# Kernel optimization log

Hardware: AMD Instinct MI355X
Metric: run time of the kernel (lower is better)

Reference implementation:

```python
import jax, jax.numpy as jnp
import numpy as np


def _rotate_half(x):
    x1, x2 = jnp.split(x, 2, axis=-1)
    return jnp.concatenate((-x2, x1), axis=-1)


def setup_inputs() -> dict:
    key = jax.random.key(0)
    ks = jax.random.split(key, 8)
    B, T, C, H = 2, 2048, 1024, 16
    Dh = C // H
    x = jax.random.normal(ks[0], (B, T, C), dtype=jnp.float32)
    # RoPE tables (T, head_dim)
    inv_freq = 1.0 / (10000.0 ** (np.arange(0, Dh, 2, dtype=np.float32) / Dh))
    pos = np.arange(T, dtype=np.float32)
    freqs = np.einsum('t,f->tf', pos, inv_freq)
    emb = np.concatenate([freqs, freqs], axis=-1)
    cos = jnp.asarray(np.cos(emb), dtype=jnp.float32)
    sin = jnp.asarray(np.sin(emb), dtype=jnp.float32)
    # causal mask: 1 where attending allowed, 0 elsewhere
    mask = jnp.tril(jnp.ones((T, T), dtype=jnp.int32))
    s = 0.02
    Wq = jax.random.normal(ks[1], (C, C), dtype=jnp.float32) * s
    Wk = jax.random.normal(ks[2], (C, C), dtype=jnp.float32) * s
    Wv = jax.random.normal(ks[3], (C, C), dtype=jnp.float32) * s
    Wo = jax.random.normal(ks[4], (C, C), dtype=jnp.float32) * s
    return {"x": x, "cos": cos, "sin": sin, "mask": mask, "n_heads": H,
            "Wq": Wq, "Wk": Wk, "Wv": Wv, "Wo": Wo}


def reference(x, cos, sin, mask, n_heads, Wq, Wk, Wv, Wo):
    B, T, C = x.shape
    H = n_heads
    Dh = C // H
    scale = Dh ** (-0.5)
    # projections (torch Linear: x @ W.T), reshape to (B, H, T, Dh)
    def proj(W):
        return (x @ W.T).reshape(B, T, H, Dh).transpose(0, 2, 1, 3)
    q, k, v = proj(Wq), proj(Wk), proj(Wv)
    # RoPE: cos/sin broadcast as (1, 1, T, Dh)
    c = cos[None, None]
    s = sin[None, None]
    q = q * c + _rotate_half(q) * s
    k = k * c + _rotate_half(k) * s
    att = jnp.einsum('bhtd,bhsd->bhts', q, k) * scale
    att = jnp.where(mask == 0, -jnp.inf, att)
    att = jax.nn.softmax(att, axis=-1)
    out = jnp.einsum('bhts,bhsd->bhtd', att, v)
    out = out.transpose(0, 2, 1, 3).reshape(B, T, C)
    return out @ Wo.T
```

## Files before the change

### kernel.cpp

```cpp
#include <hip/hip_runtime.h>
#include <stdint.h>

#define B_   2
#define T_   2048
#define C_   1024
#define H_   16
#define BT   4096
#define KDIM 1024

typedef unsigned short u16;
typedef __attribute__((ext_vector_type(8))) __bf16 bf16v8;
typedef __attribute__((ext_vector_type(4))) float f32x4;
typedef __attribute__((ext_vector_type(16))) float f32x16;
typedef __attribute__((ext_vector_type(4))) unsigned int u32x4;
typedef __attribute__((ext_vector_type(2))) unsigned int u32x2;

#define MFMA16(a, b, c) __builtin_amdgcn_mfma_f32_16x16x32_bf16((a), (b), (c), 0, 0, 0)
#define MFMA32(a, b, c) __builtin_amdgcn_mfma_f32_32x32x16_bf16((a), (b), (c), 0, 0, 0)

#define BARRIER() do { asm volatile("" ::: "memory"); \
                       __builtin_amdgcn_s_barrier();  \
                       asm volatile("" ::: "memory"); } while (0)

__device__ __forceinline__ u16 f2bf(float f) {
  __bf16 h = (__bf16)f;
  union { __bf16 h; u16 u; } v; v.h = h;
  return v.u;
}
__device__ __forceinline__ float bf2f(u16 u) {
  union { uint32_t u; float f; } v; v.u = (uint32_t)u << 16;
  return v.f;
}

__device__ __forceinline__ void xhalf(uint32_t a, uint32_t b,
                                      uint32_t& lo, uint32_t& hi) {
#if defined(__has_builtin) && __has_builtin(__builtin_amdgcn_permlane32_swap)
  u32x2 r = __builtin_amdgcn_permlane32_swap(a, b, false, false);
  lo = r.x; hi = r.y;
#else
  const bool upper = (threadIdx.x & 32) != 0;
  lo = upper ? __shfl_xor(b, 32) : a;
  hi = upper ? b : __shfl_xor(a, 32);
#endif
}

__device__ __forceinline__ void gload16(const void* g, void* l) {
  __builtin_amdgcn_global_load_lds((__attribute__((address_space(1))) void*)g,
                                   (__attribute__((address_space(3))) void*)l,
                                   16, 0, 0);
}

__global__ __launch_bounds__(256) void cvt_all(
    const float* __restrict__ x,
    const float* __restrict__ wq, const float* __restrict__ wk,
    const float* __restrict__ wv, const float* __restrict__ wo,
    u16* __restrict__ xb, u16* __restrict__ qkv_dst, u16* __restrict__ o_dst) {
  const int bid = blockIdx.x;
  const float* src;
  u16* dst;
  int i;
  if (bid < 4096) {
    src = x; dst = xb;
    i = (bid * 256 + threadIdx.x) * 4;
  } else {
    const int b2 = bid - 4096;
    const int sel = b2 >> 10;
    src = (sel == 0) ? wq : (sel == 1) ? wk : (sel == 2) ? wv : wo;
    dst = (sel < 3) ? (qkv_dst + sel * 1048576) : o_dst;
    i = ((b2 & 1023) * 256 + threadIdx.x) * 4;
  }
  float4 v = *(const float4*)(src + i);
  ushort4 o;
  o.x = f2bf(v.x); o.y = f2bf(v.y); o.z = f2bf(v.z); o.w = f2bf(v.w);
  *(ushort4*)(dst + i) = o;
}

__global__ __launch_bounds__(256, 2) void gemm_qkv32(
    const u16* __restrict__ A, const u16* __restrict__ Bm,
    u16* __restrict__ qo, u16* __restrict__ ko, u16* __restrict__ vt,
    const float* __restrict__ cosT, const float* __restrict__ sinT)
{
  __shared__ __align__(16) char smem[32768];
  const int tid = threadIdx.x;
  const int lane = tid & 63;
  const int w = tid >> 6;
  const int wm = w >> 1, wn = w & 1;
  const int lmod = lane & 15, ldiv = lane >> 4;

  const int x = blockIdx.x & 7;
  const int i = blockIdx.x >> 3;
  const int by = (x >> 1) * 8 + (i % 8);
  const int bx = (x & 1) * 12 + (i / 8);
  const int row0 = by * 128, col0 = bx * 128;

  const int ldst = (tid & 192) * 16;

  auto stage = [&](int buf, int t) {
    const int kb = t * 64;
#pragma unroll
    for (int c = 0; c < 2; ++c) {
      const int chunk = c * 256 + tid;
      const int row = chunk >> 2;
      const int col = ((chunk & 3) * 16) ^ ((row & 3) << 4);
      gload16((const char*)A + (size_t)(row0 + row) * 2048 + kb + col,
              smem + buf * 8192 + c * 4096 + ldst);
      gload16((const char*)Bm + (size_t)(col0 + row) * 2048 + kb + col,
              smem + 16384 + buf * 8192 + c * 4096 + ldst);
    }
  };

  f32x4 acc[4][4] = {};
  stage(0, 0);

  for (int t = 0; t < 32; ++t) {
    const int cur = t & 1;
    BARRIER();
    if (t + 1 < 32) {
      stage(cur ^ 1, t + 1);
      asm volatile("s_waitcnt vmcnt(4)" ::: "memory");
    } else {
      asm volatile("s_waitcnt vmcnt(0)" ::: "memory");
    }
    BARRIER();

    bf16v8 af[4], bfr[4];
#pragma unroll
    for (int mf = 0; mf < 4; ++mf) {
      const int rr = wm * 64 + mf * 16 + lmod;
      af[mf] = *(const bf16v8*)(smem + cur * 8192 + rr * 64 +
                    ((ldiv * 16) ^ ((rr & 3) << 4)));
    }
#pragma unroll
    for (int nf = 0; nf < 4; ++nf) {
      const int rr = wn * 64 + nf * 16 + lmod;
      bfr[nf] = *(const bf16v8*)(smem + 16384 + cur * 8192 + rr * 64 +
                    ((ldiv * 16) ^ ((rr & 3) << 4)));
    }
#pragma unroll
    for (int mf = 0; mf < 4; ++mf)
#pragma unroll
      for (int nf = 0; nf < 4; ++nf)
        acc[mf][nf] = MFMA16(af[mf], bfr[nf], acc[mf][nf]);
  }

  const int nb = col0 + wn * 64;
  const int proj = nb >> 10;
  const int hh = (nb & 1023) >> 6;
  if (proj < 2) {
    u16* dst = proj ? ko : qo;
#pragma unroll
    for (int mf = 0; mf < 4; ++mf) {
#pragma unroll
      for (int r = 0; r < 4; ++r) {
        const int m = row0 + wm * 64 + mf * 16 + ldiv * 4 + r;
        const int b = m >> 11, t = m & 2047;
        u16* drow = dst + ((size_t)(b * H_ + hh) * T_ + t) * 64;
#pragma unroll
        for (int nf = 0; nf < 4; ++nf) {
          const int d = nf * 16 + lmod;
          const float cs = cosT[t * 64 + d];
          const float sn = sinT[t * 64 + d];
          const float other = (nf < 2) ? acc[mf][nf + 2][r] : acc[mf][nf - 2][r];
          float val = (nf < 2) ? (acc[mf][nf][r] * cs - other * sn)
                               : (acc[mf][nf][r] * cs + other * sn);
          if (proj == 0) val *= 0.18033688011112042f;
          drow[d] = f2bf(val);
        }
      }
    }
  } else {
    BARRIER();
    char* scr = smem + w * 8192;
#pragma unroll
    for (int nf = 0; nf < 4; ++nf)
#pragma unroll
      for (int mf = 0; mf < 4; ++mf)
#pragma unroll
        for (int rp = 0; rp < 2; ++rp) {
          const int dd = nf * 16 + lmod;
          const int t0 = mf * 16 + ldiv * 4 + rp * 2;
          const uint32_t pk = (uint32_t)f2bf(acc[mf][nf][rp * 2]) |
                              ((uint32_t)f2bf(acc[mf][nf][rp * 2 + 1]) << 16);
          *(uint32_t*)(scr + ((dd * 128 + t0 * 2) ^ ((dd & 7) << 4))) = pk;
        }
    __syncthreads();
    const int trow = row0 + wm * 64;
    const int bb = trow >> 11, tl = trow & 2047;
#pragma unroll
    for (int j = 0; j < 8; ++j) {
      const int dd = j * 8 + (lane >> 3);
      const int c = lane & 7;
      const u32x4 vv = *(const u32x4*)(scr + ((dd * 128 + c * 16) ^ ((dd & 7) << 4)));
      u16* drow = vt + ((size_t)((bb * H_ + hh) * 64 + dd)) * T_ + tl;
      *(u32x4*)((char*)drow + c * 16) = vv;
    }
  }
}

template<int NN>
__global__ __launch_bounds__(256, 2) void gemm128(
    const u16* __restrict__ A, const u16* __restrict__ Bm,
    float* __restrict__ Cf)
{
  __shared__ __align__(16) u16 As[2][128 * 64];
  __shared__ __align__(16) u16 Bs[2][128 * 64];
  const int tid = threadIdx.x;
  const int lane = tid & 63;
  const int w = tid >> 6;
  const int wm = w >> 1, wn = w & 1;
  const int lmod = lane & 15, ldiv = lane >> 4;

  const int x = blockIdx.x & 7;
  const int i = blockIdx.x >> 3;
  const int by = x * 4 + (i % 4);
  const int bx = i / 4;
  const int row0 = by * 128, col0 = bx * 128;

  const int srow = tid >> 3;
  const int sswz = ((tid & 7) * 16) ^ ((srow & 7) << 4);
  const char* Abase = (const char*)A + (size_t)(row0 + srow) * (KDIM * 2) + sswz;
  const char* Bbase = (const char*)Bm + (size_t)(col0 + srow) * (KDIM * 2) + sswz;
  const int ldst = (tid & 192) * 16;

  auto stage = [&](int buf, int t) {
    const int kb = t * 128;
#pragma unroll
    for (int c = 0; c < 4; ++c)
      gload16(Abase + (size_t)c * 32 * (KDIM * 2) + kb,
              (char*)As[buf] + c * 4096 + ldst);
#pragma unroll
    for (int c = 0; c < 4; ++c)
      gload16(Bbase + (size_t)c * 32 * (KDIM * 2) + kb,
              (char*)Bs[buf] + c * 4096 + ldst);
  };

  f32x4 acc[4][4] = {};
  stage(0, 0);

  for (int t = 0; t < KDIM / 64; ++t) {
    const int cur = t & 1;
    BARRIER();
    if (t + 1 < KDIM / 64) {
      stage(cur ^ 1, t + 1);
      asm volatile("s_waitcnt vmcnt(8)" ::: "memory");
    } else {
      asm volatile("s_waitcnt vmcnt(0)" ::: "memory");
    }
    BARRIER();

    bf16v8 af[4][2], bfr[4][2];
#pragma unroll
    for (int mf = 0; mf < 4; ++mf) {
      const int rr = wm * 64 + mf * 16 + lmod;
#pragma unroll
      for (int kc = 0; kc < 2; ++kc)
        af[mf][kc] = *(const bf16v8*)((const char*)As[cur] + rr * 128 +
                          ((kc * 64 + ldiv * 16) ^ ((rr & 7) << 4)));
    }
#pragma unroll
    for (int nf = 0; nf < 4; ++nf) {
      const int rr = wn * 64 + nf * 16 + lmod;
#pragma unroll
      for (int kc = 0; kc < 2; ++kc)
        bfr[nf][kc] = *(const bf16v8*)((const char*)Bs[cur] + rr * 128 +
                          ((kc * 64 + ldiv * 16) ^ ((rr & 7) << 4)));
    }
#pragma unroll
    for (int kc = 0; kc < 2; ++kc)
#pragma unroll
      for (int mf = 0; mf < 4; ++mf)
#pragma unroll
        for (int nf = 0; nf < 4; ++nf)
          acc[mf][nf] = MFMA16(af[mf][kc], bfr[nf][kc], acc[mf][nf]);
  }

#pragma unroll
  for (int mf = 0; mf < 4; ++mf) {
    const int mbase = row0 + wm * 64 + mf * 16 + ldiv * 4;
#pragma unroll
    for (int nf = 0; nf < 4; ++nf) {
      const int n = col0 + wn * 64 + nf * 16 + lmod;
#pragma unroll
      for (int r = 0; r < 4; ++r)
        Cf[(size_t)(mbase + r) * NN + n] = acc[mf][nf][r];
    }
  }
}

__global__ __launch_bounds__(256, 2) void attn_fwd4(
    const u16* __restrict__ Q, const u16* __restrict__ K,
    const u16* __restrict__ Vt, u16* __restrict__ O,
    u16* __restrict__ part_o, float* __restrict__ pml)
{
  __shared__ __align__(16) u16 Kl[2][64 * 64];
  __shared__ __align__(16) u16 Vl[2][64 * 64];
  static const int rmap[24] = {7, 22, 23, 20, 21, 6, 18, 19, 16, 17, 5, 14,
                               15, 12, 13, 4, 10, 11, 8, 9, 3, 2, 1, 0};
  const int xcd = blockIdx.x & 7;
  const int i   = blockIdx.x >> 3;
  const int bh  = xcd * 4 + (i & 3);
  const int r   = rmap[i >> 2];
  int qb0, t0, t1, sid;
  if (r < 8) {
    qb0 = r * 128; t0 = 0; t1 = 2 * r + 2; sid = -1;
  } else {
    const int s = r - 8;
    const int c = 8 + (s >> 1);
    const int half = s & 1;
    qb0 = c * 128;
    t0 = half * (c + 1); t1 = t0 + (c + 1);
    sid = (bh * 8 + (c - 8)) * 2 + half;
  }

  const int tid = threadIdx.x, lane = tid & 63, w = tid >> 6;
  const int l31 = lane & 31, hi = lane >> 5;
  const int qrow = qb0 + w * 32;

  bf16v8 qf[4];
  {
    const u16* qp = Q + ((size_t)bh * T_ + qrow + l31) * 64 + hi * 8;
    qf[0] = *(const bf16v8*)(qp);
    qf[1] = *(const bf16v8*)(qp + 16);
    qf[2] = *(const bf16v8*)(qp + 32);
    qf[3] = *(const bf16v8*)(qp + 48);
  }

  float m2 = -1e30f, lsum = 0.f;
  f32x16 oacc0 = {}, oacc1 = {};

  const int scolb = (tid & 7) * 16;
  const int ldst = (tid & 192) * 16;

  auto stage = [&](int buf, int t) {
    const int s0 = t << 6;
#pragma unroll
    for (int c = 0; c < 2; ++c) {
      const int row = (c * 256 + tid) >> 3;
      const int sw = scolb ^ ((row & 7) << 4);
      gload16((const char*)(K + ((size_t)bh * T_ + s0 + row) * 64) + sw,
              (char*)Kl[buf] + c * 4096 + ldst);
    }
#pragma unroll
    for (int c = 0; c < 2; ++c) {
      const int row = (c * 256 + tid) >> 3;
      const int sw = scolb ^ ((row & 7) << 4);
      gload16((const char*)(Vt + ((size_t)(bh * 64 + row)) * T_ + s0) + sw,
              (char*)Vl[buf] + c * 4096 + ldst);
    }
  };

  auto substep = [&](int cur, int sub, int s0_sub) {
    bf16v8 kf[4], vf[4];
#pragma unroll
    for (int c = 0; c < 4; ++c) {
      const int row = sub * 32 + l31;
      kf[c] = *(const bf16v8*)((const char*)Kl[cur] + row * 128 +
                  ((c * 32 + hi * 16) ^ ((row & 7) << 4)));
    }
#pragma unroll
    for (int db = 0; db < 2; ++db)
#pragma unroll
      for (int kg = 0; kg < 2; ++kg) {
        const int row = db * 32 + l31;
        vf[db * 2 + kg] = *(const bf16v8*)((const char*)Vl[cur] + row * 128 +
                  ((sub * 64 + kg * 32 + hi * 16) ^ ((row & 7) << 4)));
      }
    f32x16 s = {};
    s = MFMA32(kf[0], qf[0], s);
    s = MFMA32(kf[1], qf[1], s);
    s = MFMA32(kf[2], qf[2], s);
    s = MFMA32(kf[3], qf[3], s);
    if (s0_sub + 31 > qrow) {
#pragma unroll
      for (int r2 = 0; r2 < 16; ++r2) {
        const int key = s0_sub + (r2 & 3) + 8 * (r2 >> 2) + 4 * hi;
        if (key > qrow + l31) s[r2] = -1e30f;
      }
    }
    float t8[8];
#pragma unroll
    for (int r2 = 0; r2 < 8; ++r2) t8[r2] = fmaxf(s[r2], s[r2 + 8]);
    float t4a = fmaxf(t8[0], t8[4]), t4b = fmaxf(t8[1], t8[5]);
    float t4c = fmaxf(t8[2], t8[6]), t4d = fmaxf(t8[3], t8[7]);
    float pmax = fmaxf(fmaxf(t4a, t4b), fmaxf(t4c, t4d));
    {
      uint32_t lo, hh2;
      xhalf(__builtin_bit_cast(uint32_t, pmax), __builtin_bit_cast(uint32_t, pmax), lo, hh2);
      pmax = fmaxf(__builtin_bit_cast(float, lo), __builtin_bit_cast(float, hh2));
    }
    if (!__all(pmax <= m2 + 11.5416f)) {
      const float mnew = fmaxf(m2, pmax);
      const float rs = __builtin_amdgcn_exp2f(m2 - mnew);
      lsum *= rs;
#pragma unroll
      for (int r2 = 0; r2 < 16; ++r2) { oacc0[r2] *= rs; oacc1[r2] *= rs; }
      m2 = mnew;
    }
    float p[16];
#pragma unroll
    for (int r2 = 0; r2 < 16; ++r2) p[r2] = __builtin_amdgcn_exp2f(s[r2] - m2);
    float a8[8];
#pragma unroll
    for (int r2 = 0; r2 < 8; ++r2) a8[r2] = p[r2] + p[r2 + 8];
    float a4a = a8[0] + a8[4], a4b = a8[1] + a8[5];
    float a4c = a8[2] + a8[6], a4d = a8[3] + a8[7];
    float ts = (a4a + a4b) + (a4c + a4d);
    {
      uint32_t lo, hh2;
      xhalf(__builtin_bit_cast(uint32_t, ts), __builtin_bit_cast(uint32_t, ts), lo, hh2);
      ts = __builtin_bit_cast(float, lo) + __builtin_bit_cast(float, hh2);
    }
    lsum += ts;
    uint32_t o[8];
#pragma unroll
    for (int jj = 0; jj < 8; ++jj) {
      const int r0 = 4 * (jj >> 1) + 2 * (jj & 1);
      uint32_t d;
      asm("v_cvt_pk_bf16_f32 %0, %1, %2" : "=v"(d) : "v"(p[r0]), "v"(p[r0 + 1]));
      o[jj] = d;
    }
#pragma unroll
    for (int kg = 0; kg < 2; ++kg) {
      uint32_t f0, f1, f2, f3;
      xhalf(o[4 * kg + 0], o[4 * kg + 2], f0, f2);
      xhalf(o[4 * kg + 1], o[4 * kg + 3], f1, f3);
      u32x4 fr;
      fr.x = f0; fr.y = f1; fr.z = f2; fr.w = f3;
      const bf16v8 pf = __builtin_bit_cast(bf16v8, fr);
      oacc0 = MFMA32(vf[kg], pf, oacc0);
      oacc1 = MFMA32(vf[2 + kg], pf, oacc1);
    }
  };

  stage(0, t0);
  for (int t = t0; t < t1; ++t) {
    const int cur = (t - t0) & 1;
    BARRIER();
    if (t + 1 < t1) {
      stage(cur ^ 1, t + 1);
      asm volatile("s_waitcnt vmcnt(4)" ::: "memory");
    } else {
      asm volatile("s_waitcnt vmcnt(0)" ::: "memory");
    }
    BARRIER();
#pragma unroll
    for (int sub = 0; sub < 2; ++sub) {
      const int s0_sub = t * 64 + sub * 32;
      if (s0_sub <= qrow + 31) substep(cur, sub, s0_sub);
    }
  }

  BARRIER();
  char* scr = (char*)Kl + w * 4096;
  const float inv = (sid < 0) ? (1.f / lsum) : 1.f;
#pragma unroll
  for (int r2 = 0; r2 < 8; ++r2) {
    const int r = r2 * 2;
    const int dd = (r & 3) + 8 * (r >> 2) + 4 * hi;
    const uint32_t pk0 = (uint32_t)f2bf(oacc0[r] * inv) |
                         ((uint32_t)f2bf(oacc0[r + 1] * inv) << 16);
    *(uint32_t*)(scr + ((l31 * 128 + dd * 2) ^ ((l31 & 7) << 4))) = pk0;
    const uint32_t pk1 = (uint32_t)f2bf(oacc1[r] * inv) |
                         ((uint32_t)f2bf(oacc1[r + 1] * inv) << 16);
    *(uint32_t*)(scr + ((l31 * 128 + (dd + 32) * 2) ^ ((l31 & 7) << 4))) = pk1;
  }
  __syncthreads();
  const int qq = lane >> 1, cc = lane & 1;
  if (sid < 0) {
    const int b = bh >> 4, hh = bh & 15;
    u16* orow = O + ((size_t)(b * T_ + qrow + qq)) * C_ + hh * 64 + cc * 32;
#pragma unroll
    for (int jj = 0; jj < 4; ++jj) {
      const u32x4 vv = *(const u32x4*)(scr + ((qq * 128 + cc * 64 + jj * 16) ^ ((qq & 7) << 4)));
      *(u32x4*)((char*)orow + jj * 16) = vv;
    }
  } else {
    u16* prow = part_o + ((size_t)(sid * 128 + w * 32 + qq)) * 64 + cc * 32;
#pragma unroll
    for (int jj = 0; jj < 4; ++jj) {
      const u32x4 vv = *(const u32x4*)(scr + ((qq * 128 + cc * 64 + jj * 16) ^ ((qq & 7) << 4)));
      *(u32x4*)((char*)prow + jj * 16) = vv;
    }
    if (lane < 32) {
      pml[sid * 256 + w * 32 + lane] = m2;
      pml[sid * 256 + 128 + w * 32 + lane] = lsum;
    }
  }
}

__global__ __launch_bounds__(256) void attn_combine(
    const u16* __restrict__ part_o, const float* __restrict__ pml,
    u16* __restrict__ O)
{
  const int combo = blockIdx.x;
  const int bh = combo >> 3, c8 = combo & 7;
  const int sid0 = (bh * 8 + c8) * 2;
  const int row = threadIdx.x >> 1, dh = threadIdx.x & 1;
  const float m0 = pml[sid0 * 256 + row];
  const float l0 = pml[sid0 * 256 + 128 + row];
  const float m1 = pml[(sid0 + 1) * 256 + row];
  const float l1 = pml[(sid0 + 1) * 256 + 128 + row];
  const float m = fmaxf(m0, m1);
  const float s0 = __builtin_amdgcn_exp2f(m0 - m);
  const float s1 = __builtin_amdgcn_exp2f(m1 - m);
  const float inv = 1.f / (l0 * s0 + l1 * s1);
  const u16* p0 = part_o + ((size_t)(sid0 * 128 + row)) * 64 + dh * 32;
  const u16* p1 = part_o + ((size_t)((sid0 + 1) * 128 + row)) * 64 + dh * 32;
  const int b = bh >> 4, hh = bh & 15;
  const int t = (8 + c8) * 128 + row;
  u16* dst = O + ((size_t)(b * T_ + t)) * C_ + hh * 64 + dh * 32;
#pragma unroll
  for (int j0 = 0; j0 < 4; ++j0) {
    const u32x4 a = *(const u32x4*)(p0 + j0 * 8);
    const u32x4 bq = *(const u32x4*)(p1 + j0 * 8);
    const u16* pa = (const u16*)&a;
    const u16* pb = (const u16*)&bq;
    u16 outv[8];
#pragma unroll
    for (int j = 0; j < 8; ++j)
      outv[j] = f2bf((bf2f(pa[j]) * s0 + bf2f(pb[j]) * s1) * inv);
    *(u32x4*)(dst + j0 * 8) = *(const u32x4*)outv;
  }
}

extern "C" void kernel_launch(void* const* d_in, const int* in_sizes, int n_in,
                              void* d_out, int out_size, void* d_ws, size_t ws_size,
                              hipStream_t stream) {
  const float* x    = (const float*)d_in[0];
  const float* cosT = (const float*)d_in[1];
  const float* sinT = (const float*)d_in[2];
  const float* Wq = (const float*)d_in[5];
  const float* Wk = (const float*)d_in[6];
  const float* Wv = (const float*)d_in[7];
  const float* Wo = (const float*)d_in[8];
  float* out = (float*)d_out;

  char* ws = (char*)d_ws;
  u16* xb   = (u16*)(ws);
  u16* wqkv = (u16*)(ws + 8388608);
  u16* wo   = (u16*)(ws + 14680064);
  u16* q    = (u16*)(ws + 16777216);
  u16* k    = (u16*)(ws + 25165824);
  u16* vt   = (u16*)(ws + 33554432);
  u16* aout = (u16*)(ws + 41943040);
  u16* part_o = xb;
  float* pml  = (float*)(ws + 8388608);

  cvt_all<<<8192, 256, 0, stream>>>(x, Wq, Wk, Wv, Wo, xb, wqkv, wo);

  gemm_qkv32<<<768, 256, 0, stream>>>(xb, wqkv, q, k, vt, cosT, sinT);
  attn_fwd4<<<768, 256, 0, stream>>>(q, k, vt, aout, part_o, pml);
  attn_combine<<<256, 256, 0, stream>>>(part_o, pml, aout);
  gemm128<1024><<<256, 256, 0, stream>>>(aout, wo, out);
}
```

Measured before the change: 104.5 us.

## Process both 32-key subtiles jointly in one online-softmax step with MFMA priority

When both 32-key halves of a 64-key tile are needed, the kernel now computes both QK^T blocks first, then does one combined max/rescale/exp/sum pass before the two PV MFMA groups. This halves the cross-lane reductions and rescale checks per tile and gives the scheduler more independent MFMA work to overlap with the exp math. It also wraps MFMA sequences in s_setprio to favour matrix issue across waves. The cost is higher register pressure from holding two score tiles, which may reduce occupancy.

```diff
diff --git a/kernel.cpp b/kernel.cpp
--- a/kernel.cpp
+++ b/kernel.cpp
@@ -349,14 +349,25 @@
     }
   };
 
-  auto substep = [&](int cur, int sub, int s0_sub) {
-    bf16v8 kf[4], vf[4];
-#pragma unroll
-    for (int c = 0; c < 4; ++c) {
-      const int row = sub * 32 + l31;
+  auto qk32 = [&](int cur, int sub) -> f32x16 {
+    bf16v8 kf[4];
+    const int row = sub * 32 + l31;
+#pragma unroll
+    for (int c = 0; c < 4; ++c)
       kf[c] = *(const bf16v8*)((const char*)Kl[cur] + row * 128 +
                   ((c * 32 + hi * 16) ^ ((row & 7) << 4)));
-    }
+    f32x16 s = {};
+    __builtin_amdgcn_s_setprio(1);
+    s = MFMA32(kf[0], qf[0], s);
+    s = MFMA32(kf[1], qf[1], s);
+    s = MFMA32(kf[2], qf[2], s);
+    s = MFMA32(kf[3], qf[3], s);
+    __builtin_amdgcn_s_setprio(0);
+    return s;
+  };
+
+  auto pv32 = [&](int cur, int sub, const float* p) {
+    bf16v8 vf[4];
 #pragma unroll
     for (int db = 0; db < 2; ++db)
 #pragma unroll
@@ -365,11 +376,42 @@
         vf[db * 2 + kg] = *(const bf16v8*)((const char*)Vl[cur] + row * 128 +
                   ((sub * 64 + kg * 32 + hi * 16) ^ ((row & 7) << 4)));
       }
-    f32x16 s = {};
-    s = MFMA32(kf[0], qf[0], s);
-    s = MFMA32(kf[1], qf[1], s);
-    s = MFMA32(kf[2], qf[2], s);
-    s = MFMA32(kf[3], qf[3], s);
+    uint32_t o[8];
+#pragma unroll
+    for (int jj = 0; jj < 8; ++jj) {
+      const int r0 = 4 * (jj >> 1) + 2 * (jj & 1);
+      uint32_t d;
+      asm("v_cvt_pk_bf16_f32 %0, %1, %2" : "=v"(d) : "v"(p[r0]), "v"(p[r0 + 1]));
+      o[jj] = d;
+    }
+#pragma unroll
+    for (int kg = 0; kg < 2; ++kg) {
+      uint32_t f0, f1, f2, f3;
+      xhalf(o[4 * kg + 0], o[4 * kg + 2], f0, f2);
+      xhalf(o[4 * kg + 1], o[4 * kg + 3], f1, f3);
+      u32x4 fr;
+      fr.x = f0; fr.y = f1; fr.z = f2; fr.w = f3;
+      const bf16v8 pf = __builtin_bit_cast(bf16v8, fr);
+      __builtin_amdgcn_s_setprio(1);
+      oacc0 = MFMA32(vf[kg], pf, oacc0);
+      oacc1 = MFMA32(vf[2 + kg], pf, oacc1);
+      __builtin_amdgcn_s_setprio(0);
+    }
+  };
+
+  auto rescale_to = [&](float pmax) {
+    if (!__all(pmax <= m2 + 11.5416f)) {
+      const float mnew = fmaxf(m2, pmax);
+      const float rs = __builtin_amdgcn_exp2f(m2 - mnew);
+      lsum *= rs;
+#pragma unroll
+      for (int r2 = 0; r2 < 16; ++r2) { oacc0[r2] *= rs; oacc1[r2] *= rs; }
+      m2 = mnew;
+    }
+  };
+
+  auto substep = [&](int cur, int sub, int s0_sub) {
+    f32x16 s = qk32(cur, sub);
     if (s0_sub + 31 > qrow) {
 #pragma unroll
       for (int r2 = 0; r2 < 16; ++r2) {
@@ -388,14 +430,7 @@
       xhalf(__builtin_bit_cast(uint32_t, pmax), __builtin_bit_cast(uint32_t, pmax), lo, hh2);
       pmax = fmaxf(__builtin_bit_cast(float, lo), __builtin_bit_cast(float, hh2));
     }
-    if (!__all(pmax <= m2 + 11.5416f)) {
-      const float mnew = fmaxf(m2, pmax);
-      const float rs = __builtin_amdgcn_exp2f(m2 - mnew);
-      lsum *= rs;
-#pragma unroll
-      for (int r2 = 0; r2 < 16; ++r2) { oacc0[r2] *= rs; oacc1[r2] *= rs; }
-      m2 = mnew;
-    }
+    rescale_to(pmax);
     float p[16];
 #pragma unroll
     for (int r2 = 0; r2 < 16; ++r2) p[r2] = __builtin_amdgcn_exp2f(s[r2] - m2);
@@ -411,25 +446,54 @@
       ts = __builtin_bit_cast(float, lo) + __builtin_bit_cast(float, hh2);
     }
     lsum += ts;
-    uint32_t o[8];
-#pragma unroll
-    for (int jj = 0; jj < 8; ++jj) {
-      const int r0 = 4 * (jj >> 1) + 2 * (jj & 1);
-      uint32_t d;
-      asm("v_cvt_pk_bf16_f32 %0, %1, %2" : "=v"(d) : "v"(p[r0]), "v"(p[r0 + 1]));
-      o[jj] = d;
-    }
-#pragma unroll
-    for (int kg = 0; kg < 2; ++kg) {
-      uint32_t f0, f1, f2, f3;
-      xhalf(o[4 * kg + 0], o[4 * kg + 2], f0, f2);
-      xhalf(o[4 * kg + 1], o[4 * kg + 3], f1, f3);
-      u32x4 fr;
-      fr.x = f0; fr.y = f1; fr.z = f2; fr.w = f3;
-      const bf16v8 pf = __builtin_bit_cast(bf16v8, fr);
-      oacc0 = MFMA32(vf[kg], pf, oacc0);
-      oacc1 = MFMA32(vf[2 + kg], pf, oacc1);
-    }
+    pv32(cur, sub, p);
+  };
+
+  auto substep2 = [&](int cur, int tt) {
+    f32x16 sa = qk32(cur, 0);
+    f32x16 sb = qk32(cur, 1);
+    if (tt * 64 + 63 > qrow) {
+#pragma unroll
+      for (int r2 = 0; r2 < 16; ++r2) {
+        const int kb0 = tt * 64 + (r2 & 3) + 8 * (r2 >> 2) + 4 * hi;
+        if (kb0 > qrow + l31) sa[r2] = -1e30f;
+        if (kb0 + 32 > qrow + l31) sb[r2] = -1e30f;
+      }
+    }
+    float t8[8];
+#pragma unroll
+    for (int r2 = 0; r2 < 8; ++r2)
+      t8[r2] = fmaxf(fmaxf(sa[r2], sa[r2 + 8]), fmaxf(sb[r2], sb[r2 + 8]));
+    float t4a = fmaxf(t8[0], t8[4]), t4b = fmaxf(t8[1], t8[5]);
+    float t4c = fmaxf(t8[2], t8[6]), t4d = fmaxf(t8[3], t8[7]);
+    float pmax = fmaxf(fmaxf(t4a, t4b), fmaxf(t4c, t4d));
+    {
+      uint32_t lo, hh2;
+      xhalf(__builtin_bit_cast(uint32_t, pmax), __builtin_bit_cast(uint32_t, pmax), lo, hh2);
+      pmax = fmaxf(__builtin_bit_cast(float, lo), __builtin_bit_cast(float, hh2));
+    }
+    rescale_to(pmax);
+    float pa[16], pb[16];
+#pragma unroll
+    for (int r2 = 0; r2 < 16; ++r2) {
+      pa[r2] = __builtin_amdgcn_exp2f(sa[r2] - m2);
+      pb[r2] = __builtin_amdgcn_exp2f(sb[r2] - m2);
+    }
+    float a8[8];
+#pragma unroll
+    for (int r2 = 0; r2 < 8; ++r2)
+      a8[r2] = (pa[r2] + pa[r2 + 8]) + (pb[r2] + pb[r2 + 8]);
+    float a4a = a8[0] + a8[4], a4b = a8[1] + a8[5];
+    float a4c = a8[2] + a8[6], a4d = a8[3] + a8[7];
+    float ts = (a4a + a4b) + (a4c + a4d);
+    {
+      uint32_t lo, hh2;
+      xhalf(__builtin_bit_cast(uint32_t, ts), __builtin_bit_cast(uint32_t, ts), lo, hh2);
+      ts = __builtin_bit_cast(float, lo) + __builtin_bit_cast(float, hh2);
+    }
+    lsum += ts;
+    pv32(cur, 0, pa);
+    pv32(cur, 1, pb);
   };
 
   stage(0, t0);
@@ -443,11 +507,9 @@
       asm volatile("s_waitcnt vmcnt(0)" ::: "memory");
     }
     BARRIER();
-#pragma unroll
-    for (int sub = 0; sub < 2; ++sub) {
-      const int s0_sub = t * 64 + sub * 32;
-      if (s0_sub <= qrow + 31) substep(cur, sub, s0_sub);
-    }
+    const int s0a = t * 64, s0b = t * 64 + 32;
+    if (s0b <= qrow + 31)      substep2(cur, t);
+    else if (s0a <= qrow + 31) substep(cur, 0, s0a);
   }
 
   BARRIER();
```

Result: no change. 104.4 us (-0.1%).
